# Optimization experiments

Hardware: AMD Instinct MI355X
Metric: run time of the kernel (lower is better)

Reference implementation:

```python
import jax, jax.numpy as jnp
import numpy as np

TOP_K = 8


def setup_inputs() -> dict:
    key = jax.random.key(0)
    ks = jax.random.split(key, 10)
    B, N, F = 16, 4096, 256
    M = 4096  # memory_size
    s = 1.0 / np.sqrt(F)
    return {
        "query": jax.random.normal(ks[0], (B, N, F), jnp.float32),
        "memory_keys": jax.random.normal(ks[1], (M, F), jnp.float32),
        "memory_values": jax.random.normal(ks[2], (M, F), jnp.float32),
        "Wq": jax.random.normal(ks[3], (F, F), jnp.float32) * s,
        "bq": jnp.zeros((F,), jnp.float32),
        "W1": jax.random.normal(ks[4], (2 * F, F), jnp.float32) * (1.0 / np.sqrt(2 * F)),
        "b1": jnp.zeros((F,), jnp.float32),
        "W2": jax.random.normal(ks[5], (F, F), jnp.float32) * s,
        "b2": jnp.zeros((F,), jnp.float32),
    }


def reference(query, memory_keys, memory_values, Wq, bq, W1, b1, W2, b2):
    # query: (B, N, F)
    q = jnp.einsum("bnf,fg->bng", query, Wq) + bq
    # similarity vs memory bank: (B, N, M)
    sim = jnp.einsum("bnf,mf->bnm", q, memory_keys)
    topk_sim, topk_idx = jax.lax.top_k(sim, TOP_K)          # (B, N, K)
    topk_values = memory_values[topk_idx]                    # (B, N, K, F) gather
    weights = jax.nn.softmax(topk_sim, axis=-1)[..., None]   # (B, N, K, 1)
    retrieved = jnp.sum(topk_values * weights, axis=-2)      # (B, N, F)
    h = jnp.concatenate([query, retrieved], axis=-1)         # (B, N, 2F)
    h = jax.nn.relu(jnp.einsum("bnf,fg->bng", h, W1) + b1)
    out = jnp.einsum("bnf,fg->bng", h, W2) + b2
    return out
```

## Files before the change

### kernel.cpp

```cpp
#include <hip/hip_runtime.h>

typedef _Float16 f16x8 __attribute__((ext_vector_type(8)));
typedef float f32x4 __attribute__((ext_vector_type(4)));

#define BN   65536
#define MSZ  4096
#define TOPK 8

#define MFMA(a, b, c) __builtin_amdgcn_mfma_f32_16x16x32_f16(a, b, c, 0, 0, 0)

__device__ __forceinline__ int swz2(int r, int cb) {
    return (r << 9) + (cb ^ ((((r >> 3) ^ r) & 7) << 4));
}

__global__ void prep(const float* __restrict__ keys, _Float16* __restrict__ keysSW,
                     const float* __restrict__ Wq, _Float16* __restrict__ WqT,
                     const float* __restrict__ W1, _Float16* __restrict__ W1T,
                     const float* __restrict__ W2, _Float16* __restrict__ W2T) {
    const int b = blockIdx.x, tid = threadIdx.x;
    if (b < 512) {
        int g = b * 256 + tid;
        int k = g >> 5, f8 = g & 31;
        float4 x = *(const float4*)(keys + (size_t)k * 256 + f8 * 8);
        float4 y = *(const float4*)(keys + (size_t)k * 256 + f8 * 8 + 4);
        f16x8 h = {(_Float16)x.x, (_Float16)x.y, (_Float16)x.z, (_Float16)x.w,
                   (_Float16)y.x, (_Float16)y.y, (_Float16)y.z, (_Float16)y.w};
        *(f16x8*)((char*)keysSW + ((size_t)(k >> 6) << 15) + swz2(k & 63, f8 * 16)) = h;
    } else if (b < 768) {
        int i = (b - 512) * 256 + tid;
        int kk = i >> 8, n = i & 255;
        WqT[n * 256 + kk] = (_Float16)Wq[i];
    } else if (b < 1280) {
        int i = (b - 768) * 256 + tid;
        int kk = i >> 8, n = i & 255;
        W1T[n * 512 + kk] = (_Float16)W1[i];
    } else {
        int i = (b - 1280) * 256 + tid;
        int kk = i >> 8, n = i & 255;
        W2T[n * 256 + kk] = (_Float16)W2[i];
    }
}

__device__ __forceinline__ unsigned pack_key(float s, unsigned inv12) {
    unsigned u = __float_as_uint(s);
    unsigned m = (unsigned)(((int)u) >> 31) | 0x80000000u;
    unsigned k = u ^ m;
    return (k & 0xFFFFF000u) | inv12;
}

__device__ __forceinline__ unsigned med3u(unsigned a, unsigned b, unsigned c) {
    unsigned d;
    asm("v_med3_u32 %0, %1, %2, %3" : "=v"(d) : "v"(a), "v"(b), "v"(c));
    return d;
}

template <int N>
__device__ __forceinline__ void ins(unsigned* t, unsigned key) {
#pragma unroll
    for (int p = N - 1; p > 0; --p) t[p] = med3u(t[p - 1], t[p], key);
    t[0] = (t[0] > key) ? t[0] : key;
}

__device__ __forceinline__ void load_lds16(const void* g, void* l) {
    __builtin_amdgcn_global_load_lds(
        (const __attribute__((address_space(1))) unsigned int*)g,
        (__attribute__((address_space(3))) unsigned int*)l, 16, 0, 0);
}

__global__ __launch_bounds__(256, 2) void fused_all(
        const float*    __restrict__ query,
        const _Float16* __restrict__ keysSW,
        const float*    __restrict__ vals,
        const _Float16* __restrict__ WqT,
        const float*    __restrict__ bq,
        const _Float16* __restrict__ W1T,
        const float*    __restrict__ b1,
        const _Float16* __restrict__ W2T,
        const float*    __restrict__ b2,
        float* __restrict__ out)
{
    __shared__ __attribute__((aligned(16))) unsigned char SM[65536];
    unsigned char* const SA = SM;
    unsigned char* const SB = SM + 32768;

    const int tid  = threadIdx.x;
    const int lane = tid & 63, quad = lane >> 4, l16 = lane & 15, wave = tid >> 6;
    const size_t row0 = (size_t)blockIdx.x * 64;

#pragma unroll
    for (int j = 0; j < 8; ++j) {
        int u = (j << 8) + tid;
        int r = u >> 5, f = (u & 31) << 3;
        float4 x = *(const float4*)(query + (row0 + r) * 256 + f);
        float4 y = *(const float4*)(query + (row0 + r) * 256 + f + 4);
        f16x8 h = {(_Float16)x.x, (_Float16)x.y, (_Float16)x.z, (_Float16)x.w,
                   (_Float16)y.x, (_Float16)y.y, (_Float16)y.z, (_Float16)y.w};
        *(f16x8*)(SA + swz2(r, f << 1)) = h;
    }
    __syncthreads();

    {
        f32x4 acc[4][4];
#pragma unroll
        for (int rt = 0; rt < 4; ++rt)
#pragma unroll
            for (int nt = 0; nt < 4; ++nt)
                acc[rt][nt] = (f32x4){0.f, 0.f, 0.f, 0.f};
#pragma unroll
        for (int kf = 0; kf < 8; ++kf) {
            f16x8 a[4];
#pragma unroll
            for (int rt = 0; rt < 4; ++rt)
                a[rt] = *(const f16x8*)(SA + swz2(rt * 16 + l16, kf * 64 + quad * 16));
#pragma unroll
            for (int nt = 0; nt < 4; ++nt) {
                int n0 = wave * 16 + nt * 64;
                f16x8 b = *(const f16x8*)(WqT + (size_t)(n0 + l16) * 256 + kf * 32 + quad * 8);
#pragma unroll
                for (int rt = 0; rt < 4; ++rt)
                    acc[rt][nt] = MFMA(a[rt], b, acc[rt][nt]);
            }
        }
#pragma unroll
        for (int nt = 0; nt < 4; ++nt) {
            int col = wave * 16 + nt * 64 + l16;
            float bv = bq[col];
#pragma unroll
            for (int rt = 0; rt < 4; ++rt)
#pragma unroll
                for (int r = 0; r < 4; ++r) {
                    int row = rt * 16 + quad * 4 + r;
                    *(_Float16*)(SB + swz2(row, col * 2)) =
                        (_Float16)(acc[rt][nt][r] + bv);
                }
        }
    }
    __syncthreads();

    f16x8 af0[8], af1[8];
    {
        const char* src = (const char*)keysSW + wave * 8192;
        char* dst = (char*)SA + wave * 8192;
#pragma unroll
        for (int j = 0; j < 8; ++j)
            load_lds16(src + j * 1024 + lane * 16, dst + j * 1024);
#pragma unroll
        for (int nk = 0; nk < 8; ++nk) {
            af0[nk] = *(const f16x8*)(SB + swz2((wave & 1) * 32 + l16,      nk * 64 + quad * 16));
            af1[nk] = *(const f16x8*)(SB + swz2((wave & 1) * 32 + 16 + l16, nk * 64 + quad * 16));
        }
    }
    __syncthreads();

    unsigned tk[8][6];
#pragma unroll
    for (int s = 0; s < 8; ++s)
#pragma unroll
        for (int e = 0; e < 6; ++e) tk[s][e] = 0u;

    const int kh = (wave >> 1) * 32;

#pragma unroll 1
    for (int t = 0; t < 64; ++t) {
        unsigned char* cur = SM + ((t & 1) << 15);
        unsigned char* nxt = SM + (((t + 1) & 1) << 15);
        {
            const char* src = (const char*)keysSW + ((size_t)((t + 1) & 63) << 15) + wave * 8192;
            char* dst = (char*)nxt + wave * 8192;
#pragma unroll
            for (int j = 0; j < 8; ++j)
                load_lds16(src + j * 1024 + lane * 16, dst + j * 1024);
        }
#pragma unroll
        for (int c = 0; c < 2; ++c) {
            const int kl = kh + c * 16;
            f16x8 bf[8];
#pragma unroll
            for (int nk = 0; nk < 8; ++nk)
                bf[nk] = *(const f16x8*)(cur + swz2(kl + l16, nk * 64 + quad * 16));
            f32x4 a0 = {0.f, 0.f, 0.f, 0.f};
            f32x4 a1 = {0.f, 0.f, 0.f, 0.f};
#pragma unroll
            for (int nk = 0; nk < 8; ++nk) {
                a0 = MFMA(af0[nk], bf[nk], a0);
                a1 = MFMA(af1[nk], bf[nk], a1);
            }
            unsigned inv = (~(unsigned)((t << 6) + kl + l16)) & 0xFFFu;
#pragma unroll
            for (int r = 0; r < 4; ++r) ins<6>(tk[r],     pack_key(a0[r], inv));
#pragma unroll
            for (int r = 0; r < 4; ++r) ins<6>(tk[4 + r], pack_key(a1[r], inv));
        }
        __syncthreads();
    }

    unsigned m4[4][7];
    {
        const int kb = l16 & 1;
#pragma unroll
        for (int j = 0; j < 4; ++j) {
#pragma unroll
            for (int e = 0; e < 6; ++e) m4[j][e] = kb ? tk[4 + j][e] : tk[j][e];
            m4[j][6] = 0u;
#pragma unroll
            for (int e = 0; e < 6; ++e) {
                unsigned snd = kb ? tk[j][e] : tk[4 + j][e];
                ins<7>(m4[j], __shfl_xor(snd, 1));
            }
        }
    }
    unsigned m2[2][8];
    {
        const int k2 = (l16 >> 1) & 1;
#pragma unroll
        for (int j = 0; j < 2; ++j) {
#pragma unroll
            for (int e = 0; e < 7; ++e) m2[j][e] = k2 ? m4[2 + j][e] : m4[j][e];
            m2[j][7] = 0u;
#pragma unroll
            for (int e = 0; e < 7; ++e) {
                unsigned snd = k2 ? m4[j][e] : m4[2 + j][e];
                ins<8>(m2[j], __shfl_xor(snd, 2));
            }
        }
    }
    unsigned fm[8];
    {
        const int k3 = (l16 >> 2) & 1;
        unsigned oth[8];
#pragma unroll
        for (int e = 0; e < 8; ++e) {
            fm[e]  = k3 ? m2[1][e] : m2[0][e];
            oth[e] = k3 ? m2[0][e] : m2[1][e];
        }
#pragma unroll
        for (int e = 0; e < 8; ++e) ins<8>(fm, __shfl_xor(oth[e], 4));
    }
    {
        unsigned rcv[8];
#pragma unroll
        for (int e = 0; e < 8; ++e) rcv[e] = __shfl_xor(fm[e], 8);
#pragma unroll
        for (int e = 0; e < 8; ++e) ins<8>(fm, rcv[e]);
    }
    if (l16 < 8) {
        const int rl  = quad * 4 + 2 * ((l16 >> 1) & 1) + ((l16 >> 2) & 1) + 16 * (l16 & 1);
        const int row = (wave & 1) * 32 + rl;
        unsigned* Mrg = (unsigned*)SA;
#pragma unroll
        for (int e = 0; e < 8; ++e) Mrg[((wave >> 1) * 64 + row) * 8 + e] = fm[e];
    }
    __syncthreads();

    const int rmap = ((wave & 1) << 5) + ((wave & 2) << 3);
    int idx[8];
    {
        const unsigned* Mrg = (const unsigned*)SA;
        const int row = rmap + l16;
        unsigned f[8];
#pragma unroll
        for (int e = 0; e < 8; ++e) f[e] = Mrg[row * 8 + e];
#pragma unroll
        for (int e = 0; e < 8; ++e) ins<8>(f, Mrg[(64 + row) * 8 + e]);
#pragma unroll
        for (int e = 0; e < 8; ++e) idx[e] = 4095 - (int)(f[e] & 0xFFFu);
    }

    float wt[8];
    {
        f16x8 afr[8];
        const bool hi = (wave & 2) != 0;
#pragma unroll
        for (int nk = 0; nk < 8; ++nk) afr[nk] = hi ? af1[nk] : af0[nk];
        float ps[8];
#pragma unroll
        for (int e = 0; e < 8; ++e) {
            const unsigned char* kb =
                (const unsigned char*)keysSW + ((size_t)(idx[e] >> 6) << 15);
            const int kr = idx[e] & 63;
            float s = 0.f;
#pragma unroll
            for (int nk = 0; nk < 8; ++nk) {
                f16x8 kv = *(const f16x8*)(kb + swz2(kr, nk * 64 + quad * 16));
                f16x8 qv = afr[nk];
#pragma unroll
                for (int i = 0; i < 8; ++i) s += (float)qv[i] * (float)kv[i];
            }
            ps[e] = s;
        }
#pragma unroll
        for (int e = 0; e < 8; ++e) {
            ps[e] += __shfl_xor(ps[e], 16);
            ps[e] += __shfl_xor(ps[e], 32);
        }
        float mx = ps[0];
#pragma unroll
        for (int e = 1; e < 8; ++e) mx = fmaxf(mx, ps[e]);
        float z = 0.f;
#pragma unroll
        for (int e = 0; e < 8; ++e) { wt[e] = __expf(ps[e] - mx); z += wt[e]; }
        float rz = 1.f / z;
#pragma unroll
        for (int e = 0; e < 8; ++e) wt[e] *= rz;
    }

    {
        float rv[64];
#pragma unroll
        for (int i = 0; i < 64; ++i) rv[i] = 0.f;
#pragma unroll
        for (int e = 0; e < 8; ++e) {
            const float4* vp = (const float4*)(vals + (size_t)(idx[e] & (MSZ - 1)) * 256 + quad * 64);
            float w = wt[e];
#pragma unroll
            for (int j = 0; j < 16; ++j) {
                float4 v = vp[j];
                rv[j * 4 + 0] += w * v.x; rv[j * 4 + 1] += w * v.y;
                rv[j * 4 + 2] += w * v.z; rv[j * 4 + 3] += w * v.w;
            }
        }
        const int row = rmap + l16;
#pragma unroll
        for (int j = 0; j < 8; ++j) {
            f16x8 h = {(_Float16)rv[j * 8 + 0], (_Float16)rv[j * 8 + 1],
                       (_Float16)rv[j * 8 + 2], (_Float16)rv[j * 8 + 3],
                       (_Float16)rv[j * 8 + 4], (_Float16)rv[j * 8 + 5],
                       (_Float16)rv[j * 8 + 6], (_Float16)rv[j * 8 + 7]};
            *(f16x8*)(SB + swz2(row, quad * 128 + (j << 4))) = h;
        }
    }
    __syncthreads();

#pragma unroll
    for (int j = 0; j < 8; ++j) {
        int u = (j << 8) + tid;
        int r = u >> 5, f = (u & 31) << 3;
        float4 x = *(const float4*)(query + (row0 + r) * 256 + f);
        float4 y = *(const float4*)(query + (row0 + r) * 256 + f + 4);
        f16x8 h = {(_Float16)x.x, (_Float16)x.y, (_Float16)x.z, (_Float16)x.w,
                   (_Float16)y.x, (_Float16)y.y, (_Float16)y.z, (_Float16)y.w};
        *(f16x8*)(SA + swz2(r, f << 1)) = h;
    }
    __syncthreads();

    {
        f32x4 acc[4][4];
#pragma unroll
        for (int rt = 0; rt < 4; ++rt)
#pragma unroll
            for (int nt = 0; nt < 4; ++nt)
                acc[rt][nt] = (f32x4){0.f, 0.f, 0.f, 0.f};
#pragma unroll
        for (int kf = 0; kf < 16; ++kf) {
            const unsigned char* base = (kf < 8) ? SA : SB;
            const int cb = (kf & 7) * 64 + quad * 16;
            f16x8 a[4];
#pragma unroll
            for (int rt = 0; rt < 4; ++rt)
                a[rt] = *(const f16x8*)(base + swz2(rt * 16 + l16, cb));
#pragma unroll
            for (int nt = 0; nt < 4; ++nt) {
                int n0 = wave * 16 + nt * 64;
                f16x8 b = *(const f16x8*)(W1T + (size_t)(n0 + l16) * 512 + kf * 32 + quad * 8);
#pragma unroll
                for (int rt = 0; rt < 4; ++rt)
                    acc[rt][nt] = MFMA(a[rt], b, acc[rt][nt]);
            }
        }
        __syncthreads();
#pragma unroll
        for (int nt = 0; nt < 4; ++nt) {
            int col = wave * 16 + nt * 64 + l16;
            float bv = b1[col];
#pragma unroll
            for (int rt = 0; rt < 4; ++rt)
#pragma unroll
                for (int r = 0; r < 4; ++r) {
                    int row = rt * 16 + quad * 4 + r;
                    *(_Float16*)(SA + swz2(row, col * 2)) =
                        (_Float16)fmaxf(acc[rt][nt][r] + bv, 0.f);
                }
        }
    }
    __syncthreads();

    {
        f32x4 acc[4][4];
#pragma unroll
        for (int rt = 0; rt < 4; ++rt)
#pragma unroll
            for (int nt = 0; nt < 4; ++nt)
                acc[rt][nt] = (f32x4){0.f, 0.f, 0.f, 0.f};
#pragma unroll
        for (int kf = 0; kf < 8; ++kf) {
            f16x8 a[4];
#pragma unroll
            for (int rt = 0; rt < 4; ++rt)
                a[rt] = *(const f16x8*)(SA + swz2(rt * 16 + l16, kf * 64 + quad * 16));
#pragma unroll
            for (int nt = 0; nt < 4; ++nt) {
                int n0 = wave * 16 + nt * 64;
                f16x8 b = *(const f16x8*)(W2T + (size_t)(n0 + l16) * 256 + kf * 32 + quad * 8);
#pragma unroll
                for (int rt = 0; rt < 4; ++rt)
                    acc[rt][nt] = MFMA(a[rt], b, acc[rt][nt]);
            }
        }
#pragma unroll
        for (int nt = 0; nt < 4; ++nt) {
            int col = wave * 16 + nt * 64 + l16;
            float bv = b2[col];
#pragma unroll
            for (int rt = 0; rt < 4; ++rt)
#pragma unroll
                for (int r = 0; r < 4; ++r)
                    out[(row0 + rt * 16 + quad * 4 + r) * 256 + col] =
                        acc[rt][nt][r] + bv;
        }
    }
}

extern "C" void kernel_launch(void* const* d_in, const int* in_sizes, int n_in,
                              void* d_out, int out_size, void* d_ws, size_t ws_size,
                              hipStream_t stream) {
    const float* query = (const float*)d_in[0];
    const float* keys  = (const float*)d_in[1];
    const float* vals  = (const float*)d_in[2];
    const float* Wq    = (const float*)d_in[3];
    const float* bq    = (const float*)d_in[4];
    const float* W1    = (const float*)d_in[5];
    const float* b1    = (const float*)d_in[6];
    const float* W2    = (const float*)d_in[7];
    const float* b2    = (const float*)d_in[8];
    float* out = (float*)d_out;

    char* ws = (char*)d_ws;
    _Float16* keysSW = (_Float16*)(ws);
    _Float16* WqT    = (_Float16*)(ws + 2097152);
    _Float16* W1T    = (_Float16*)(ws + 2097152 + 131072);
    _Float16* W2T    = (_Float16*)(ws + 2097152 + 131072 + 262144);

    prep<<<1536, 256, 0, stream>>>(keys, keysSW, Wq, WqT, W1, W1T, W2, W2T);

    fused_all<<<BN / 64, 256, 0, stream>>>(query, keysSW, vals, WqT, bq,
                                           W1T, b1, W2T, b2, out);
}
```

Before: 484.7 us.

## Shrink LDS footprint to raise occupancy, halve key tiles, pre-tile weights for MFMA

Cuts shared memory from 64KB to 36KB by reusing one region for all stages. The key stream now moves in 32-row double-buffered tiles over 128 iterations, with each wave handling 16 keys. The kernel targets 3 waves per EU. Weights are stored pre-tiled in the MFMA B-fragment order so each lane does one contiguous 16-byte load. The W1 product is split so the retrieved half is done before the query is reloaded. The aim is higher occupancy and coalesced weight loads, at the cost of more barriers per key tile and tighter register limits.

```diff
diff --git a/kernel.cpp b/kernel.cpp
--- a/kernel.cpp
+++ b/kernel.cpp
@@ -14,9 +14,9 @@
 }
 
 __global__ void prep(const float* __restrict__ keys, _Float16* __restrict__ keysSW,
-                     const float* __restrict__ Wq, _Float16* __restrict__ WqT,
-                     const float* __restrict__ W1, _Float16* __restrict__ W1T,
-                     const float* __restrict__ W2, _Float16* __restrict__ W2T) {
+                     const float* __restrict__ Wq, _Float16* __restrict__ Wq2,
+                     const float* __restrict__ W1, _Float16* __restrict__ W12,
+                     const float* __restrict__ W2, _Float16* __restrict__ W22) {
     const int b = blockIdx.x, tid = threadIdx.x;
     if (b < 512) {
         int g = b * 256 + tid;
@@ -25,19 +25,22 @@
         float4 y = *(const float4*)(keys + (size_t)k * 256 + f8 * 8 + 4);
         f16x8 h = {(_Float16)x.x, (_Float16)x.y, (_Float16)x.z, (_Float16)x.w,
                    (_Float16)y.x, (_Float16)y.y, (_Float16)y.z, (_Float16)y.w};
-        *(f16x8*)((char*)keysSW + ((size_t)(k >> 6) << 15) + swz2(k & 63, f8 * 16)) = h;
+        *(f16x8*)((char*)keysSW + ((size_t)(k >> 5) << 14) + swz2(k & 31, f8 * 16)) = h;
     } else if (b < 768) {
         int i = (b - 512) * 256 + tid;
-        int kk = i >> 8, n = i & 255;
-        WqT[n * 256 + kk] = (_Float16)Wq[i];
+        int k = i >> 8, n = i & 255;
+        int d = ((n >> 4) * 8 + (k >> 5)) * 512 + (((k >> 3) & 3) * 16 + (n & 15)) * 8 + (k & 7);
+        Wq2[d] = (_Float16)Wq[i];
     } else if (b < 1280) {
         int i = (b - 768) * 256 + tid;
-        int kk = i >> 8, n = i & 255;
-        W1T[n * 512 + kk] = (_Float16)W1[i];
+        int k = i >> 8, n = i & 255;
+        int d = ((n >> 4) * 16 + (k >> 5)) * 512 + (((k >> 3) & 3) * 16 + (n & 15)) * 8 + (k & 7);
+        W12[d] = (_Float16)W1[i];
     } else {
         int i = (b - 1280) * 256 + tid;
-        int kk = i >> 8, n = i & 255;
-        W2T[n * 256 + kk] = (_Float16)W2[i];
+        int k = i >> 8, n = i & 255;
+        int d = ((n >> 4) * 8 + (k >> 5)) * 512 + (((k >> 3) & 3) * 16 + (n & 15)) * 8 + (k & 7);
+        W22[d] = (_Float16)W2[i];
     }
 }
 
@@ -67,21 +70,21 @@
         (__attribute__((address_space(3))) unsigned int*)l, 16, 0, 0);
 }
 
-__global__ __launch_bounds__(256, 2) void fused_all(
+__global__ __launch_bounds__(256) __attribute__((amdgpu_waves_per_eu(3, 3)))
+void fused_all(
         const float*    __restrict__ query,
         const _Float16* __restrict__ keysSW,
         const float*    __restrict__ vals,
-        const _Float16* __restrict__ WqT,
+        const _Float16* __restrict__ Wq2,
         const float*    __restrict__ bq,
-        const _Float16* __restrict__ W1T,
+        const _Float16* __restrict__ W12,
         const float*    __restrict__ b1,
-        const _Float16* __restrict__ W2T,
+        const _Float16* __restrict__ W22,
         const float*    __restrict__ b2,
         float* __restrict__ out)
 {
-    __shared__ __attribute__((aligned(16))) unsigned char SM[65536];
-    unsigned char* const SA = SM;
-    unsigned char* const SB = SM + 32768;
+    __shared__ __attribute__((aligned(16))) unsigned char SM[36864];
+    unsigned* const Mrg = (unsigned*)(SM + 32768);
 
     const int tid  = threadIdx.x;
     const int lane = tid & 63, quad = lane >> 4, l16 = lane & 15, wave = tid >> 6;
@@ -95,7 +98,7 @@
         float4 y = *(const float4*)(query + (row0 + r) * 256 + f + 4);
         f16x8 h = {(_Float16)x.x, (_Float16)x.y, (_Float16)x.z, (_Float16)x.w,
                    (_Float16)y.x, (_Float16)y.y, (_Float16)y.z, (_Float16)y.w};
-        *(f16x8*)(SA + swz2(r, f << 1)) = h;
+        *(f16x8*)(SM + swz2(r, f << 1)) = h;
     }
     __syncthreads();
 
@@ -111,16 +114,16 @@
             f16x8 a[4];
 #pragma unroll
             for (int rt = 0; rt < 4; ++rt)
-                a[rt] = *(const f16x8*)(SA + swz2(rt * 16 + l16, kf * 64 + quad * 16));
+                a[rt] = *(const f16x8*)(SM + swz2(rt * 16 + l16, kf * 64 + quad * 16));
 #pragma unroll
             for (int nt = 0; nt < 4; ++nt) {
-                int n0 = wave * 16 + nt * 64;
-                f16x8 b = *(const f16x8*)(WqT + (size_t)(n0 + l16) * 256 + kf * 32 + quad * 8);
+                f16x8 b = *(const f16x8*)(Wq2 + (size_t)((wave + nt * 4) * 8 + kf) * 512 + lane * 8);
 #pragma unroll
                 for (int rt = 0; rt < 4; ++rt)
                     acc[rt][nt] = MFMA(a[rt], b, acc[rt][nt]);
             }
         }
+        __syncthreads();
 #pragma unroll
         for (int nt = 0; nt < 4; ++nt) {
             int col = wave * 16 + nt * 64 + l16;
@@ -130,7 +133,7 @@
 #pragma unroll
                 for (int r = 0; r < 4; ++r) {
                     int row = rt * 16 + quad * 4 + r;
-                    *(_Float16*)(SB + swz2(row, col * 2)) =
+                    *(_Float16*)(SM + swz2(row, col * 2)) =
                         (_Float16)(acc[rt][nt][r] + bv);
                 }
         }
@@ -139,16 +142,20 @@
 
     f16x8 af0[8], af1[8];
     {
-        const char* src = (const char*)keysSW + wave * 8192;
-        char* dst = (char*)SA + wave * 8192;
-#pragma unroll
-        for (int j = 0; j < 8; ++j)
-            load_lds16(src + j * 1024 + lane * 16, dst + j * 1024);
+        const int ag = (wave & 1) * 32;
 #pragma unroll
         for (int nk = 0; nk < 8; ++nk) {
-            af0[nk] = *(const f16x8*)(SB + swz2((wave & 1) * 32 + l16,      nk * 64 + quad * 16));
-            af1[nk] = *(const f16x8*)(SB + swz2((wave & 1) * 32 + 16 + l16, nk * 64 + quad * 16));
-        }
+            af0[nk] = *(const f16x8*)(SM + swz2(ag + l16,      nk * 64 + quad * 16));
+            af1[nk] = *(const f16x8*)(SM + swz2(ag + 16 + l16, nk * 64 + quad * 16));
+        }
+    }
+    __syncthreads();
+
+    {
+        const char* src = (const char*)keysSW + wave * 4096;
+#pragma unroll
+        for (int j = 0; j < 4; ++j)
+            load_lds16(src + j * 1024 + lane * 16, (char*)SM + wave * 4096 + j * 1024);
     }
     __syncthreads();
 
@@ -158,39 +165,34 @@
 #pragma unroll
         for (int e = 0; e < 6; ++e) tk[s][e] = 0u;
 
-    const int kh = (wave >> 1) * 32;
+    const int kl = (wave >> 1) * 16;
 
 #pragma unroll 1
-    for (int t = 0; t < 64; ++t) {
-        unsigned char* cur = SM + ((t & 1) << 15);
-        unsigned char* nxt = SM + (((t + 1) & 1) << 15);
+    for (int t = 0; t < 128; ++t) {
+        unsigned char* cur = SM + ((t & 1) << 14);
+        unsigned char* nxt = SM + (((t + 1) & 1) << 14);
         {
-            const char* src = (const char*)keysSW + ((size_t)((t + 1) & 63) << 15) + wave * 8192;
-            char* dst = (char*)nxt + wave * 8192;
-#pragma unroll
-            for (int j = 0; j < 8; ++j)
-                load_lds16(src + j * 1024 + lane * 16, dst + j * 1024);
-        }
-#pragma unroll
-        for (int c = 0; c < 2; ++c) {
-            const int kl = kh + c * 16;
-            f16x8 bf[8];
-#pragma unroll
-            for (int nk = 0; nk < 8; ++nk)
-                bf[nk] = *(const f16x8*)(cur + swz2(kl + l16, nk * 64 + quad * 16));
-            f32x4 a0 = {0.f, 0.f, 0.f, 0.f};
-            f32x4 a1 = {0.f, 0.f, 0.f, 0.f};
-#pragma unroll
-            for (int nk = 0; nk < 8; ++nk) {
-                a0 = MFMA(af0[nk], bf[nk], a0);
-                a1 = MFMA(af1[nk], bf[nk], a1);
-            }
-            unsigned inv = (~(unsigned)((t << 6) + kl + l16)) & 0xFFFu;
-#pragma unroll
-            for (int r = 0; r < 4; ++r) ins<6>(tk[r],     pack_key(a0[r], inv));
-#pragma unroll
-            for (int r = 0; r < 4; ++r) ins<6>(tk[4 + r], pack_key(a1[r], inv));
-        }
+            const char* src = (const char*)keysSW + ((size_t)((t + 1) & 127) << 14) + wave * 4096;
+#pragma unroll
+            for (int j = 0; j < 4; ++j)
+                load_lds16(src + j * 1024 + lane * 16, (char*)nxt + wave * 4096 + j * 1024);
+        }
+        f16x8 bf[8];
+#pragma unroll
+        for (int nk = 0; nk < 8; ++nk)
+            bf[nk] = *(const f16x8*)(cur + swz2(kl + l16, nk * 64 + quad * 16));
+        f32x4 a0 = {0.f, 0.f, 0.f, 0.f};
+        f32x4 a1 = {0.f, 0.f, 0.f, 0.f};
+#pragma unroll
+        for (int nk = 0; nk < 8; ++nk) {
+            a0 = MFMA(af0[nk], bf[nk], a0);
+            a1 = MFMA(af1[nk], bf[nk], a1);
+        }
+        unsigned inv = (~(unsigned)((t << 5) + kl + l16)) & 0xFFFu;
+#pragma unroll
+        for (int r = 0; r < 4; ++r) ins<6>(tk[r],     pack_key(a0[r], inv));
+#pragma unroll
+        for (int r = 0; r < 4; ++r) ins<6>(tk[4 + r], pack_key(a1[r], inv));
         __syncthreads();
     }
 
@@ -246,7 +248,6 @@
     if (l16 < 8) {
         const int rl  = quad * 4 + 2 * ((l16 >> 1) & 1) + ((l16 >> 2) & 1) + 16 * (l16 & 1);
         const int row = (wave & 1) * 32 + rl;
-        unsigned* Mrg = (unsigned*)SA;
 #pragma unroll
         for (int e = 0; e < 8; ++e) Mrg[((wave >> 1) * 64 + row) * 8 + e] = fm[e];
     }
@@ -255,7 +256,6 @@
     const int rmap = ((wave & 1) << 5) + ((wave & 2) << 3);
     int idx[8];
     {
-        const unsigned* Mrg = (const unsigned*)SA;
         const int row = rmap + l16;
         unsigned f[8];
 #pragma unroll
@@ -276,8 +276,8 @@
 #pragma unroll
         for (int e = 0; e < 8; ++e) {
             const unsigned char* kb =
-                (const unsigned char*)keysSW + ((size_t)(idx[e] >> 6) << 15);
-            const int kr = idx[e] & 63;
+                (const unsigned char*)keysSW + ((size_t)(idx[e] >> 5) << 14);
+            const int kr = idx[e] & 31;
             float s = 0.f;
 #pragma unroll
             for (int nk = 0; nk < 8; ++nk) {
@@ -326,7 +326,29 @@
                        (_Float16)rv[j * 8 + 2], (_Float16)rv[j * 8 + 3],
                        (_Float16)rv[j * 8 + 4], (_Float16)rv[j * 8 + 5],
                        (_Float16)rv[j * 8 + 6], (_Float16)rv[j * 8 + 7]};
-            *(f16x8*)(SB + swz2(row, quad * 128 + (j << 4))) = h;
+            *(f16x8*)(SM + swz2(row, quad * 128 + (j << 4))) = h;
+        }
+    }
+    __syncthreads();
+
+    f32x4 acc[4][4];
+#pragma unroll
+    for (int rt = 0; rt < 4; ++rt)
+#pragma unroll
+        for (int nt = 0; nt < 4; ++nt)
+            acc[rt][nt] = (f32x4){0.f, 0.f, 0.f, 0.f};
+#pragma unroll
+    for (int kf = 0; kf < 8; ++kf) {
+        f16x8 a[4];
+#pragma unroll
+        for (int rt = 0; rt < 4; ++rt)
+            a[rt] = *(const f16x8*)(SM + swz2(rt * 16 + l16, kf * 64 + quad * 16));
+#pragma unroll
+        for (int nt = 0; nt < 4; ++nt) {
+            f16x8 b = *(const f16x8*)(W12 + (size_t)((wave + nt * 4) * 16 + 8 + kf) * 512 + lane * 8);
+#pragma unroll
+            for (int rt = 0; rt < 4; ++rt)
+                acc[rt][nt] = MFMA(a[rt], b, acc[rt][nt]);
         }
     }
     __syncthreads();
@@ -339,29 +361,20 @@
         float4 y = *(const float4*)(query + (row0 + r) * 256 + f + 4);
         f16x8 h = {(_Float16)x.x, (_Float16)x.y, (_Float16)x.z, (_Float16)x.w,
                    (_Float16)y.x, (_Float16)y.y, (_Float16)y.z, (_Float16)y.w};
-        *(f16x8*)(SA + swz2(r, f << 1)) = h;
-    }
-    __syncthreads();
-
-    {
-        f32x4 acc[4][4];
-#pragma unroll
-        for (int rt = 0; rt < 4; ++rt)
-#pragma unroll
-            for (int nt = 0; nt < 4; ++nt)
-                acc[rt][nt] = (f32x4){0.f, 0.f, 0.f, 0.f};
-#pragma unroll
-        for (int kf = 0; kf < 16; ++kf) {
-            const unsigned char* base = (kf < 8) ? SA : SB;
-            const int cb = (kf & 7) * 64 + quad * 16;
+        *(f16x8*)(SM + swz2(r, f << 1)) = h;
+    }
+    __syncthreads();
+
+    {
+#pragma unroll
+        for (int kf = 0; kf < 8; ++kf) {
             f16x8 a[4];
 #pragma unroll
             for (int rt = 0; rt < 4; ++rt)
-                a[rt] = *(const f16x8*)(base + swz2(rt * 16 + l16, cb));
+                a[rt] = *(const f16x8*)(SM + swz2(rt * 16 + l16, kf * 64 + quad * 16));
 #pragma unroll
             for (int nt = 0; nt < 4; ++nt) {
-                int n0 = wave * 16 + nt * 64;
-                f16x8 b = *(const f16x8*)(W1T + (size_t)(n0 + l16) * 512 + kf * 32 + quad * 8);
+                f16x8 b = *(const f16x8*)(W12 + (size_t)((wave + nt * 4) * 16 + kf) * 512 + lane * 8);
 #pragma unroll
                 for (int rt = 0; rt < 4; ++rt)
                     acc[rt][nt] = MFMA(a[rt], b, acc[rt][nt]);
@@ -377,7 +390,7 @@
 #pragma unroll
                 for (int r = 0; r < 4; ++r) {
                     int row = rt * 16 + quad * 4 + r;
-                    *(_Float16*)(SA + swz2(row, col * 2)) =
+                    *(_Float16*)(SM + swz2(row, col * 2)) =
                         (_Float16)fmaxf(acc[rt][nt][r] + bv, 0.f);
                 }
         }
@@ -385,25 +398,24 @@
     __syncthreads();
 
     {
-        f32x4 acc[4][4];
+        f32x4 acc2[4][4];
 #pragma unroll
         for (int rt = 0; rt < 4; ++rt)
 #pragma unroll
             for (int nt = 0; nt < 4; ++nt)
-                acc[rt][nt] = (f32x4){0.f, 0.f, 0.f, 0.f};
+                acc2[rt][nt] = (f32x4){0.f, 0.f, 0.f, 0.f};
 #pragma unroll
         for (int kf = 0; kf < 8; ++kf) {
             f16x8 a[4];
 #pragma unroll
             for (int rt = 0; rt < 4; ++rt)
-                a[rt] = *(const f16x8*)(SA + swz2(rt * 16 + l16, kf * 64 + quad * 16));
+                a[rt] = *(const f16x8*)(SM + swz2(rt * 16 + l16, kf * 64 + quad * 16));
 #pragma unroll
             for (int nt = 0; nt < 4; ++nt) {
-                int n0 = wave * 16 + nt * 64;
-                f16x8 b = *(const f16x8*)(W2T + (size_t)(n0 + l16) * 256 + kf * 32 + quad * 8);
+                f16x8 b = *(const f16x8*)(W22 + (size_t)((wave + nt * 4) * 8 + kf) * 512 + lane * 8);
 #pragma unroll
                 for (int rt = 0; rt < 4; ++rt)
-                    acc[rt][nt] = MFMA(a[rt], b, acc[rt][nt]);
+                    acc2[rt][nt] = MFMA(a[rt], b, acc2[rt][nt]);
             }
         }
 #pragma unroll
@@ -415,7 +427,7 @@
 #pragma unroll
                 for (int r = 0; r < 4; ++r)
                     out[(row0 + rt * 16 + quad * 4 + r) * 256 + col] =
-                        acc[rt][nt][r] + bv;
+                        acc2[rt][nt][r] + bv;
         }
     }
 }
@@ -436,12 +448,12 @@
 
     char* ws = (char*)d_ws;
     _Float16* keysSW = (_Float16*)(ws);
-    _Float16* WqT    = (_Float16*)(ws + 2097152);
-    _Float16* W1T    = (_Float16*)(ws + 2097152 + 131072);
-    _Float16* W2T    = (_Float16*)(ws + 2097152 + 131072 + 262144);
-
-    prep<<<1536, 256, 0, stream>>>(keys, keysSW, Wq, WqT, W1, W1T, W2, W2T);
-
-    fused_all<<<BN / 64, 256, 0, stream>>>(query, keysSW, vals, WqT, bq,
-                                           W1T, b1, W2T, b2, out);
-}
+    _Float16* Wq2    = (_Float16*)(ws + 2097152);
+    _Float16* W12    = (_Float16*)(ws + 2097152 + 131072);
+    _Float16* W22    = (_Float16*)(ws + 2097152 + 131072 + 262144);
+
+    prep<<<1536, 256, 0, stream>>>(keys, keysSW, Wq, Wq2, W1, W12, W2, W22);
+
+    fused_all<<<BN / 64, 256, 0, stream>>>(query, keysSW, vals, Wq2, bq,
+                                           W12, b1, W22, b2, out);
+}
```

Result: slower. 523.7 us (+8.0%).
